# Performance work log

Measured on AMD Instinct MI355X. Metric: run time of the kernel, lower is better.

## Reference

```python
import jax, jax.numpy as jnp
import numpy as np

HEAD_DIM = 64
AGGR = 4  # attn_aggr_ratio
BN_EPS = 1e-5


def _conv1x1(x, W, b=None):
    # x: [N, Cin, L], W: [Cout, Cin] -> [N, Cout, L]
    y = jnp.einsum('ncl,oc->nol', x, W)
    if b is not None:
        y = y + b[None, :, None]
    return y


def _bn(x, gamma, beta, mean, var):
    # BatchNorm1d, eval mode (running stats). x: [N, C, L]
    inv = gamma * jax.lax.rsqrt(var + BN_EPS)
    return x * inv[None, :, None] + (beta - mean * inv)[None, :, None]


def setup_inputs() -> dict:
    key = jax.random.key(0)
    ks = jax.random.split(key, 8)
    N, C, L = 4, 256, 4096
    s = 1.0 / np.sqrt(C)
    inp = {
        'x': jax.random.normal(ks[0], (N, C, L), jnp.float32),
        'Wq': jax.random.normal(ks[1], (C, C), jnp.float32) * s,
        'bq': jnp.zeros((C,), jnp.float32),
        'Wk': jax.random.normal(ks[2], (C, C), jnp.float32) * s,
        'bk': jnp.zeros((C,), jnp.float32),
        'Wv': jax.random.normal(ks[3], (C, C), jnp.float32) * s,
        'bv': jnp.zeros((C,), jnp.float32),
        'Wo': jax.random.normal(ks[4], (C, C), jnp.float32) * s,
        'bo': jnp.zeros((C,), jnp.float32),
        'Wa': jax.random.normal(ks[5], (C, C), jnp.float32) * s,
        'g1': jnp.ones((C,), jnp.float32), 'b1': jnp.zeros((C,), jnp.float32),
        'm1': jnp.zeros((C,), jnp.float32), 'v1': jnp.ones((C,), jnp.float32),
        'g2': jnp.ones((C,), jnp.float32), 'b2': jnp.zeros((C,), jnp.float32),
        'm2': jnp.zeros((C,), jnp.float32), 'v2': jnp.ones((C,), jnp.float32),
    }
    return inp


def reference(x, Wq, bq, Wk, bk, Wv, bv, Wo, bo, Wa,
              g1, b1, m1, v1, g2, b2, m2, v2):
    N, C, L = x.shape
    H, E = C // HEAD_DIM, HEAD_DIM
    # q projection on full-resolution input
    q = _conv1x1(x, Wq, bq).reshape(N, H, E, L)
    # LocalAwareAggregationBlock: avg+max pool (kernel=AGGR, L divisible), 1x1 conv, BN
    xp = x.reshape(N, C, L // AGGR, AGGR)
    xa = xp.mean(axis=-1) + xp.max(axis=-1)          # [N, C, L//AGGR]
    xa = _conv1x1(xa, Wa)                             # bias=False
    xa = _bn(xa, g1, b1, m1, v1)
    # post-aggregation norm
    xa = _bn(xa, g2, b2, m2, v2)
    k = _conv1x1(xa, Wk, bk).reshape(N, H, E, -1)     # [N, H, E, L2]
    v = _conv1x1(xa, Wv, bv).reshape(N, H, E, -1)
    # attention: softmax((q/sqrt(E))^T k) @ v^T
    scale = 1.0 / np.sqrt(E)
    scores = jnp.einsum('nhel,nhem->nhlm', q * scale, k)  # [N, H, L, L2]
    attn = jax.nn.softmax(scores, axis=-1)
    o = jnp.einsum('nhlm,nhem->nhel', attn, v).reshape(N, C, L)
    return _conv1x1(o, Wo, bo)
```

## Files before the change

### kernel.cpp

```cpp
#include <hip/hip_runtime.h>
#include <stdint.h>

constexpr int NBATCH = 4;
constexpr int CH     = 256;
constexpr int LEN    = 4096;
constexpr int LPOOL  = 1024;
constexpr int NH     = 4;
constexpr int HD     = 64;

typedef __attribute__((ext_vector_type(8))) short short8;
typedef __attribute__((ext_vector_type(4))) float float4e;
typedef __attribute__((ext_vector_type(16))) float float16e;
typedef __attribute__((ext_vector_type(2))) unsigned uint2v;

__device__ __forceinline__ unsigned short f2bf(float f) {
    union { unsigned int i; float f; } v; v.f = f;
    unsigned int lsb = (v.i >> 16) & 1u;
    v.i += 0x7fffu + lsb;
    return (unsigned short)(v.i >> 16);
}
__device__ __forceinline__ unsigned pack2bf(float lo, float hi) {
    unsigned a = __float_as_uint(lo) + 0x8000u;
    unsigned b = __float_as_uint(hi) + 0x8000u;
    return __builtin_amdgcn_perm(b, a, 0x07060302u);
}
__device__ __forceinline__ float fast_exp2(float x) {
#if __has_builtin(__builtin_amdgcn_exp2f)
    return __builtin_amdgcn_exp2f(x);
#else
    float r;
    asm("v_exp_f32 %0, %1" : "=v"(r) : "v"(x));
    return r;
#endif
}
__device__ __forceinline__ void gload16(const void* g, void* l) {
    __builtin_amdgcn_global_load_lds(
        (const __attribute__((address_space(1))) unsigned int*)g,
        (__attribute__((address_space(3))) unsigned int*)l, 16, 0, 0);
}

__global__ __launch_bounds__(256) void transpool_setup(
    const float* __restrict__ x, unsigned short* __restrict__ xbf,
    unsigned short* __restrict__ poolT,
    const float* __restrict__ w0, const float* __restrict__ w1,
    const float* __restrict__ w2, const float* __restrict__ w3,
    const float* __restrict__ w4, unsigned short* __restrict__ outW,
    const float* __restrict__ g1, const float* __restrict__ b1,
    const float* __restrict__ m1, const float* __restrict__ v1,
    const float* __restrict__ g2, const float* __restrict__ b2,
    const float* __restrict__ m2, const float* __restrict__ v2,
    float* __restrict__ scale, float* __restrict__ shift,
    const float* __restrict__ bk, const float* __restrict__ bv,
    float* __restrict__ bkv)
{
    __shared__ float T[64][65];
    __shared__ float P16[64][17];
    int b = blockIdx.x, t = threadIdx.x;
    if (b >= 1024) {
        int sb = b - 1024;
        if (sb < 320) {
            int gid = sb * 256 + t;
            int w = gid >> 14;
            int off = (gid & 16383) * 4;
            const float* src = (w == 0) ? w0 : (w == 1) ? w1 : (w == 2) ? w2 : (w == 3) ? w3 : w4;
            float4 v = *(const float4*)(src + off);
            uint2 pk;
            pk.x = pack2bf(v.x, v.y);
            pk.y = pack2bf(v.z, v.w);
            *(uint2*)(outW + w * 65536 + off) = pk;
        } else {
            float inv1 = g1[t] * rsqrtf(v1[t] + 1e-5f);
            float inv2 = g2[t] * rsqrtf(v2[t] + 1e-5f);
            scale[t] = inv1 * inv2;
            shift[t] = (b1[t] - m1[t] * inv1) * inv2 + (b2[t] - m2[t] * inv2);
            bkv[t] = bk[t];
            bkv[256 + t] = bv[t];
        }
        return;
    }
    int n = b >> 8, c0 = ((b >> 6) & 3) * 64, l0 = (b & 63) * 64;
    const float* xp = x + ((size_t)n * CH + c0) * LEN + l0;
    #pragma unroll
    for (int i = 0; i < 4; i++) {
        int idx = t + i * 256;
        int c = idx >> 4, l4 = idx & 15;
        float4 v = *(const float4*)(xp + (size_t)c * LEN + l4 * 4);
        T[c][l4 * 4 + 0] = v.x; T[c][l4 * 4 + 1] = v.y;
        T[c][l4 * 4 + 2] = v.z; T[c][l4 * 4 + 3] = v.w;
        P16[c][l4] = (v.x + v.y + v.z + v.w) * 0.25f
                   + fmaxf(fmaxf(v.x, v.y), fmaxf(v.z, v.w));
    }
    __syncthreads();
    unsigned short* op = xbf + ((size_t)n * LEN + l0) * CH + c0;
    #pragma unroll
    for (int i = 0; i < 4; i++) {
        int idx = t + i * 256;
        int l = idx >> 4, c4 = idx & 15;
        uint2 pk;
        pk.x = pack2bf(T[c4 * 4 + 0][l], T[c4 * 4 + 1][l]);
        pk.y = pack2bf(T[c4 * 4 + 2][l], T[c4 * 4 + 3][l]);
        *(uint2*)(op + (size_t)l * CH + c4 * 4) = pk;
    }
    int p0 = l0 >> 2;
    #pragma unroll
    for (int k = 0; k < 2; k++) {
        int p = (t >> 5) + k * 8;
        int c2 = (t & 31) * 2;
        unsigned pk = pack2bf(P16[c2][p], P16[c2 + 1][p]);
        *(unsigned*)(poolT + ((size_t)n * LPOOL + p0 + p) * CH + c0 + c2) = pk;
    }
}

__global__ __launch_bounds__(256, 4) void gemm_mfma(
    const unsigned short* __restrict__ A,
    const unsigned short* __restrict__ B, size_t bBatch,
    const float* __restrict__ biasRow,
    const float* __restrict__ scale, const float* __restrict__ shift,
    float* __restrict__ outF, size_t oFBatch,
    unsigned short* __restrict__ out1, size_t o1Batch, int cs1,
    unsigned short* __restrict__ out2, size_t o2Batch, int rs2, int rowSplit,
    int NN, float outScale)
{
    __shared__ unsigned short As[2][64 * 64];
    __shared__ unsigned short Bs[2][64 * 64];

    int n = blockIdx.z;
    int t = threadIdx.x;
    int wave = t >> 6, lane = t & 63, m = lane & 15, quad = lane >> 4;
    int wm = wave & 1, wn = wave >> 1;
    int rowTile = blockIdx.y * 64;
    int col0 = blockIdx.x * 64;

    const unsigned short* Ab = A + (size_t)rowTile * 256;
    const unsigned short* Bb = B + (size_t)n * bBatch + (size_t)col0 * 256;

    float4e acc[2][2] = {};

    int srow[2], sch[2], ldsW[2];
    #pragma unroll
    for (int i = 0; i < 2; i++) {
        int idx = t + i * 256;
        srow[i] = idx >> 3;
        sch[i]  = idx & 7;
        ldsW[i] = wave * 1024 + i * 4096;
    }

    int aoff[2][2], boff[2][2];
    #pragma unroll
    for (int i = 0; i < 2; i++) {
        int ra = wm * 32 + i * 16 + m;
        int rb = wn * 32 + i * 16 + m;
        #pragma unroll
        for (int kc = 0; kc < 2; kc++) {
            aoff[i][kc] = ra * 128 + kc * 64 + quad * 16;
            boff[i][kc] = rb * 128 + kc * 64 + quad * 16;
        }
    }

    #pragma unroll
    for (int i = 0; i < 2; i++) {
        gload16(Ab + (size_t)srow[i] * 256 + sch[i] * 8, (char*)As[0] + ldsW[i]);
        gload16(Bb + (size_t)srow[i] * 256 + sch[i] * 8, (char*)Bs[0] + ldsW[i]);
    }

    #pragma unroll
    for (int s = 0; s < 4; s++) {
        int cur = s & 1;
        asm volatile("s_waitcnt vmcnt(0)" ::: "memory");
        __builtin_amdgcn_sched_barrier(0);
        __builtin_amdgcn_s_barrier();
        __builtin_amdgcn_sched_barrier(0);
        if (s < 3) {
            int nxt = cur ^ 1;
            int kk = (s + 1) * 64;
            #pragma unroll
            for (int i = 0; i < 2; i++) {
                gload16(Ab + (size_t)srow[i] * 256 + kk + sch[i] * 8, (char*)As[nxt] + ldsW[i]);
                gload16(Bb + (size_t)srow[i] * 256 + kk + sch[i] * 8, (char*)Bs[nxt] + ldsW[i]);
            }
        }
        const char* AsC = (const char*)As[cur];
        const char* BsC = (const char*)Bs[cur];
        #pragma unroll
        for (int kc = 0; kc < 2; kc++) {
            short8 af[2], bfr[2];
            #pragma unroll
            for (int i = 0; i < 2; i++) {
                af[i]  = *(const short8*)(AsC + aoff[i][kc]);
                bfr[i] = *(const short8*)(BsC + boff[i][kc]);
            }
            __builtin_amdgcn_s_setprio(1);
            #pragma unroll
            for (int i = 0; i < 2; i++)
                #pragma unroll
                for (int j = 0; j < 2; j++)
                    acc[i][j] = __builtin_amdgcn_mfma_f32_16x16x32_bf16(af[i], bfr[j], acc[i][j], 0, 0, 0);
            __builtin_amdgcn_s_setprio(0);
        }
    }
    __syncthreads();

    if (outF) {
        float* TOf = (float*)Bs;
        float* dst = outF + (size_t)n * oFBatch;
        #pragma unroll
        for (int i = 0; i < 2; i++) {
            int rowL = wm * 32 + i * 16 + quad * 4;
            int rowG = rowTile + rowL;
            float br[4], sc[4], sh[4];
            #pragma unroll
            for (int r = 0; r < 4; r++) {
                br[r] = biasRow ? biasRow[rowG + r] : 0.0f;
                sc[r] = scale ? scale[rowG + r] : 1.0f;
                sh[r] = shift ? shift[rowG + r] : 0.0f;
            }
            #pragma unroll
            for (int j = 0; j < 2; j++) {
                int colL = wn * 32 + j * 16 + m;
                float4e c = acc[i][j];
                #pragma unroll
                for (int r = 0; r < 4; r++)
                    TOf[(rowL + r) * 64 + colL] = ((c[r] + br[r]) * sc[r] + sh[r]) * outScale;
            }
        }
        __syncthreads();
        #pragma unroll
        for (int w = 0; w < 4; w++) {
            int idx = t + w * 256;
            int row = idx >> 4, c4 = idx & 15;
            *(float4*)(dst + (size_t)(rowTile + row) * NN + col0 + c4 * 4) =
                *(const float4*)&TOf[row * 64 + c4 * 4];
        }
        return;
    }

    bool mode2 = (rowTile >= rowSplit);
    unsigned short* TO = (unsigned short*)Bs;
    #pragma unroll
    for (int i = 0; i < 2; i++) {
        int rowL = wm * 32 + i * 16 + quad * 4;
        int rowG = rowTile + rowL;
        float br[4], sc[4], sh[4];
        #pragma unroll
        for (int r = 0; r < 4; r++) {
            br[r] = biasRow ? biasRow[rowG + r] : 0.0f;
            sc[r] = scale ? scale[rowG + r] : 1.0f;
            sh[r] = shift ? shift[rowG + r] : 0.0f;
        }
        #pragma unroll
        for (int j = 0; j < 2; j++) {
            int colL = wn * 32 + j * 16 + m;
            float4e c = acc[i][j];
            float v0 = ((c[0] + br[0]) * sc[0] + sh[0]) * outScale;
            float v1 = ((c[1] + br[1]) * sc[1] + sh[1]) * outScale;
            float v2 = ((c[2] + br[2]) * sc[2] + sh[2]) * outScale;
            float v3 = ((c[3] + br[3]) * sc[3] + sh[3]) * outScale;
            if (!mode2) {
                uint2 pk;
                pk.x = pack2bf(v0, v1);
                pk.y = pack2bf(v2, v3);
                *(uint2*)&TO[colL * 72 + rowL] = pk;
            } else {
                TO[(rowL + 0) * 72 + colL] = f2bf(v0);
                TO[(rowL + 1) * 72 + colL] = f2bf(v1);
                TO[(rowL + 2) * 72 + colL] = f2bf(v2);
                TO[(rowL + 3) * 72 + colL] = f2bf(v3);
            }
        }
    }
    __syncthreads();
    if (!mode2) {
        unsigned short* dst = out1 + (size_t)n * o1Batch;
        #pragma unroll
        for (int w = 0; w < 2; w++) {
            int idx = t + w * 256;
            int l = idx >> 3, ch = idx & 7;
            *(uint4*)(dst + (size_t)(col0 + l) * cs1 + rowTile + ch * 8) =
                *(const uint4*)&TO[l * 72 + ch * 8];
        }
    } else {
        unsigned short* dst = out2 + (size_t)n * o2Batch;
        int rowBase = rowTile - rowSplit;
        #pragma unroll
        for (int w = 0; w < 2; w++) {
            int idx = t + w * 256;
            int row = idx >> 3, ch = idx & 7;
            *(uint4*)(dst + (size_t)(rowBase + row) * rs2 + col0 + ch * 8) =
                *(const uint4*)&TO[row * 72 + ch * 8];
        }
    }
}

__global__ __launch_bounds__(256, 2) void attn_mfma(
    const unsigned short* __restrict__ Qb,
    const unsigned short* __restrict__ Kb,
    const unsigned short* __restrict__ Vb,
    unsigned short* __restrict__ Obf)
{
    __shared__ unsigned short Ks[2][64 * 64];
    __shared__ unsigned short Vs[2][64 * 64];

    int qb = blockIdx.x;
    int h  = blockIdx.y;
    int n  = blockIdx.z;
    int t  = threadIdx.x;
    int wave = t >> 6, lane = t & 63;
    int col = lane & 31;
    int hi  = lane >> 5;
    int l0 = qb * 128 + wave * 32;

    const unsigned short* qp = Qb + ((size_t)n * LEN + l0 + col) * CH + h * HD + hi * 8;
    short8 bQ[4];
    #pragma unroll
    for (int dc = 0; dc < 4; dc++)
        bQ[dc] = *(const short8*)(qp + dc * 16);

    float16e Oa[2];
    #pragma unroll
    for (int e = 0; e < 2; e++)
        #pragma unroll
        for (int r = 0; r < 16; r++) Oa[e][r] = 0.0f;
    float l_run = 0.0f;

    const unsigned short* KgBase = Kb + (size_t)n * LPOOL * CH + h * HD;
    const unsigned short* VgBase = Vb + ((size_t)n * CH + h * HD) * LPOOL;
    const float NEG = -17.312340f;

    int srow[2], schs[2], ldsb[2];
    #pragma unroll
    for (int i = 0; i < 2; i++) {
        int idx = t + i * 256;
        srow[i] = idx >> 3;
        schs[i] = (idx & 7) ^ (srow[i] & 7);
        ldsb[i] = wave * 1024 + i * 4096;
    }
    int ldoff[2][4];
    #pragma unroll
    for (int g = 0; g < 2; g++)
        #pragma unroll
        for (int c = 0; c < 4; c++) {
            int row = g * 32 + col;
            ldoff[g][c] = row * 128 + ((c * 32 + hi * 16) ^ ((row & 7) << 4));
        }

    #pragma unroll
    for (int i = 0; i < 2; i++) {
        gload16(KgBase + (size_t)srow[i] * CH + schs[i] * 8, (char*)Ks[0] + ldsb[i]);
        gload16(VgBase + (size_t)srow[i] * LPOOL + schs[i] * 8, (char*)Vs[0] + ldsb[i]);
    }

    #pragma unroll 2
    for (int kt = 0; kt < 16; kt++) {
        int cur = kt & 1;
        asm volatile("s_waitcnt vmcnt(0)" ::: "memory");
        __builtin_amdgcn_sched_barrier(0);
        __builtin_amdgcn_s_barrier();
        __builtin_amdgcn_sched_barrier(0);
        if (kt < 15) {
            int nxt = cur ^ 1;
            const unsigned short* ksrc = KgBase + (size_t)(kt + 1) * 64 * CH;
            const unsigned short* vsrc = VgBase + (kt + 1) * 64;
            #pragma unroll
            for (int i = 0; i < 2; i++) {
                gload16(ksrc + (size_t)srow[i] * CH + schs[i] * 8, (char*)Ks[nxt] + ldsb[i]);
                gload16(vsrc + (size_t)srow[i] * LPOOL + schs[i] * 8, (char*)Vs[nxt] + ldsb[i]);
            }
        }

        const char* KsC = (const char*)Ks[cur];
        const char* VsC = (const char*)Vs[cur];
        #pragma unroll
        for (int kh = 0; kh < 2; kh++) {
            float16e c;
            #pragma unroll
            for (int r = 0; r < 16; r++) c[r] = NEG;
            __builtin_amdgcn_s_setprio(1);
            #pragma unroll
            for (int dc = 0; dc < 4; dc++) {
                short8 a = *(const short8*)(KsC + ldoff[kh][dc]);
                c = __builtin_amdgcn_mfma_f32_32x32x16_bf16(a, bQ[dc], c, 0, 0, 0);
            }
            __builtin_amdgcn_s_setprio(0);
            float p[16];
            #pragma unroll
            for (int r = 0; r < 16; r++) p[r] = fast_exp2(c[r]);
            l_run += ((p[0] + p[1]) + (p[2] + p[3])) + ((p[4] + p[5]) + (p[6] + p[7]))
                   + ((p[8] + p[9]) + (p[10] + p[11])) + ((p[12] + p[13]) + (p[14] + p[15]));
            union { unsigned u[4]; short8 s; } bP[2];
            #pragma unroll
            for (int kc2 = 0; kc2 < 2; kc2++) {
                int rb = kc2 * 8;
                unsigned A0 = pack2bf(p[rb + 0], p[rb + 1]);
                unsigned B0 = pack2bf(p[rb + 4], p[rb + 5]);
                unsigned A1 = pack2bf(p[rb + 2], p[rb + 3]);
                unsigned B1 = pack2bf(p[rb + 6], p[rb + 7]);
                uint2v s0 = __builtin_amdgcn_permlane32_swap(A0, B0, false, false);
                uint2v s1 = __builtin_amdgcn_permlane32_swap(A1, B1, false, false);
                bP[kc2].u[0] = s0[0];
                bP[kc2].u[1] = s1[0];
                bP[kc2].u[2] = s0[1];
                bP[kc2].u[3] = s1[1];
            }
            __builtin_amdgcn_s_setprio(1);
            #pragma unroll
            for (int eh = 0; eh < 2; eh++)
                #pragma unroll
                for (int kc2 = 0; kc2 < 2; kc2++) {
                    short8 av = *(const short8*)(VsC + ldoff[eh][kh * 2 + kc2]);
                    Oa[eh] = __builtin_amdgcn_mfma_f32_32x32x16_bf16(av, bP[kc2].s, Oa[eh], 0, 0, 0);
                }
            __builtin_amdgcn_s_setprio(0);
        }
    }

    float l = l_run + __shfl_xor(l_run, 32);
    float inv = 1.0f / l;
    unsigned short* op = Obf + ((size_t)n * LEN + l0 + col) * CH + h * HD + hi * 4;
    #pragma unroll
    for (int eh = 0; eh < 2; eh++)
        #pragma unroll
        for (int rq = 0; rq < 4; rq++) {
            int r = rq * 4;
            uint2 pk;
            pk.x = pack2bf(Oa[eh][r + 0] * inv, Oa[eh][r + 1] * inv);
            pk.y = pack2bf(Oa[eh][r + 2] * inv, Oa[eh][r + 3] * inv);
            *(uint2*)(op + eh * 32 + rq * 8) = pk;
        }
}

extern "C" void kernel_launch(void* const* d_in, const int* in_sizes, int n_in,
                              void* d_out, int out_size, void* d_ws, size_t ws_size,
                              hipStream_t stream)
{
    const float* x  = (const float*)d_in[0];
    const float* Wq = (const float*)d_in[1];
    const float* bq = (const float*)d_in[2];
    const float* Wk = (const float*)d_in[3];
    const float* bk = (const float*)d_in[4];
    const float* Wv = (const float*)d_in[5];
    const float* bv = (const float*)d_in[6];
    const float* Wo = (const float*)d_in[7];
    const float* bo = (const float*)d_in[8];
    const float* Wa = (const float*)d_in[9];
    const float* g1 = (const float*)d_in[10];
    const float* b1 = (const float*)d_in[11];
    const float* m1 = (const float*)d_in[12];
    const float* v1 = (const float*)d_in[13];
    const float* g2 = (const float*)d_in[14];
    const float* b2 = (const float*)d_in[15];
    const float* m2 = (const float*)d_in[16];
    const float* v2 = (const float*)d_in[17];

    float* wsf      = (float*)d_ws;
    float* bn_scale = wsf;
    float* bn_shift = wsf + 256;
    float* bkv      = wsf + 512;
    unsigned short* Wbf   = (unsigned short*)(wsf + 1024);
    unsigned short* xbf   = Wbf + 5 * 65536;
    unsigned short* poolT = xbf   + (size_t)NBATCH * LEN * CH;
    unsigned short* xabf  = poolT + (size_t)NBATCH * LPOOL * CH;
    unsigned short* Kbf   = xabf  + (size_t)NBATCH * LPOOL * CH;
    unsigned short* Vbf   = Kbf   + (size_t)NBATCH * LPOOL * CH;
    unsigned short* Qbf   = Vbf   + (size_t)NBATCH * LPOOL * CH;
    unsigned short* Obf   = Qbf   + (size_t)NBATCH * LEN * CH;

    transpool_setup<<<1345, 256, 0, stream>>>(x, xbf, poolT,
        Wq, Wk, Wv, Wo, Wa, Wbf,
        g1, b1, m1, v1, g2, b2, m2, v2, bn_scale, bn_shift, bk, bv, bkv);

    gemm_mfma<<<dim3(64, 4, 4), 256, 0, stream>>>(
        Wbf + 0 * 65536, xbf, (size_t)LEN * CH, bq, nullptr, nullptr,
        nullptr, 0, Qbf, (size_t)LEN * CH, 256, nullptr, 0, 0, 1 << 30,
        LEN, 0.18033688f);

    gemm_mfma<<<dim3(16, 4, 4), 256, 0, stream>>>(
        Wbf + 4 * 65536, poolT, (size_t)LPOOL * CH, nullptr, bn_scale, bn_shift,
        nullptr, 0, xabf, (size_t)LPOOL * CH, 256, nullptr, 0, 0, 1 << 30,
        LPOOL, 1.0f);

    gemm_mfma<<<dim3(16, 8, 4), 256, 0, stream>>>(
        Wbf + 1 * 65536, xabf, (size_t)LPOOL * CH, bkv, nullptr, nullptr,
        nullptr, 0, Kbf, (size_t)LPOOL * CH, 256, Vbf, (size_t)LPOOL * CH, LPOOL, 256,
        LPOOL, 1.0f);

    attn_mfma<<<dim3(LEN / 128, NH, NBATCH), 256, 0, stream>>>(Qbf, Kbf, Vbf, Obf);

    gemm_mfma<<<dim3(64, 4, 4), 256, 0, stream>>>(
        Wbf + 3 * 65536, Obf, (size_t)LEN * CH, bo, nullptr, nullptr,
        (float*)d_out, (size_t)CH * LEN, nullptr, 0, 0, nullptr, 0, 0, 1 << 30,
        LEN, 1.0f);
}
```

Before: 156.9 us.

## Fuse all stages into one persistent kernel with atomic grid barriers

```diff
diff --git a/kernel.cpp b/kernel.cpp
--- a/kernel.cpp
+++ b/kernel.cpp
@@ -7,6 +7,7 @@
 constexpr int LPOOL  = 1024;
 constexpr int NH     = 4;
 constexpr int HD     = 64;
+constexpr int NBLK   = 512;
 
 typedef __attribute__((ext_vector_type(8))) short short8;
 typedef __attribute__((ext_vector_type(4))) float float4e;
@@ -39,7 +40,19 @@
         (__attribute__((address_space(3))) unsigned int*)l, 16, 0, 0);
 }
 
-__global__ __launch_bounds__(256) void transpool_setup(
+__device__ __forceinline__ void gbar(unsigned* cnt, unsigned target) {
+    __threadfence();
+    __syncthreads();
+    if (threadIdx.x == 0) {
+        __hip_atomic_fetch_add(cnt, 1u, __ATOMIC_RELEASE, __HIP_MEMORY_SCOPE_AGENT);
+        while (__hip_atomic_load(cnt, __ATOMIC_ACQUIRE, __HIP_MEMORY_SCOPE_AGENT) < target)
+            __builtin_amdgcn_s_sleep(8);
+    }
+    __syncthreads();
+}
+
+__device__ __forceinline__ void transpool_block(
+    int b, char* smemc,
     const float* __restrict__ x, unsigned short* __restrict__ xbf,
     unsigned short* __restrict__ poolT,
     const float* __restrict__ w0, const float* __restrict__ w1,
@@ -53,9 +66,9 @@
     const float* __restrict__ bk, const float* __restrict__ bv,
     float* __restrict__ bkv)
 {
-    __shared__ float T[64][65];
-    __shared__ float P16[64][17];
-    int b = blockIdx.x, t = threadIdx.x;
+    float* T  = (float*)smemc;
+    float* P16 = (float*)(smemc + 16640);
+    int t = threadIdx.x;
     if (b >= 1024) {
         int sb = b - 1024;
         if (sb < 320) {
@@ -85,10 +98,10 @@
         int idx = t + i * 256;
         int c = idx >> 4, l4 = idx & 15;
         float4 v = *(const float4*)(xp + (size_t)c * LEN + l4 * 4);
-        T[c][l4 * 4 + 0] = v.x; T[c][l4 * 4 + 1] = v.y;
-        T[c][l4 * 4 + 2] = v.z; T[c][l4 * 4 + 3] = v.w;
-        P16[c][l4] = (v.x + v.y + v.z + v.w) * 0.25f
-                   + fmaxf(fmaxf(v.x, v.y), fmaxf(v.z, v.w));
+        T[c * 65 + l4 * 4 + 0] = v.x; T[c * 65 + l4 * 4 + 1] = v.y;
+        T[c * 65 + l4 * 4 + 2] = v.z; T[c * 65 + l4 * 4 + 3] = v.w;
+        P16[c * 17 + l4] = (v.x + v.y + v.z + v.w) * 0.25f
+                         + fmaxf(fmaxf(v.x, v.y), fmaxf(v.z, v.w));
     }
     __syncthreads();
     unsigned short* op = xbf + ((size_t)n * LEN + l0) * CH + c0;
@@ -97,8 +110,8 @@
         int idx = t + i * 256;
         int l = idx >> 4, c4 = idx & 15;
         uint2 pk;
-        pk.x = pack2bf(T[c4 * 4 + 0][l], T[c4 * 4 + 1][l]);
-        pk.y = pack2bf(T[c4 * 4 + 2][l], T[c4 * 4 + 3][l]);
+        pk.x = pack2bf(T[(c4 * 4 + 0) * 65 + l], T[(c4 * 4 + 1) * 65 + l]);
+        pk.y = pack2bf(T[(c4 * 4 + 2) * 65 + l], T[(c4 * 4 + 3) * 65 + l]);
         *(uint2*)(op + (size_t)l * CH + c4 * 4) = pk;
     }
     int p0 = l0 >> 2;
@@ -106,12 +119,13 @@
     for (int k = 0; k < 2; k++) {
         int p = (t >> 5) + k * 8;
         int c2 = (t & 31) * 2;
-        unsigned pk = pack2bf(P16[c2][p], P16[c2 + 1][p]);
+        unsigned pk = pack2bf(P16[c2 * 17 + p], P16[(c2 + 1) * 17 + p]);
         *(unsigned*)(poolT + ((size_t)n * LPOOL + p0 + p) * CH + c0 + c2) = pk;
     }
 }
 
-__global__ __launch_bounds__(256, 4) void gemm_mfma(
+__device__ __forceinline__ void gemm_block(
+    int bx, int by, int bz, char* smemc,
     const unsigned short* __restrict__ A,
     const unsigned short* __restrict__ B, size_t bBatch,
     const float* __restrict__ biasRow,
@@ -121,15 +135,15 @@
     unsigned short* __restrict__ out2, size_t o2Batch, int rs2, int rowSplit,
     int NN, float outScale)
 {
-    __shared__ unsigned short As[2][64 * 64];
-    __shared__ unsigned short Bs[2][64 * 64];
-
-    int n = blockIdx.z;
+    char* AsB[2] = { smemc,         smemc + 8192 };
+    char* BsB[2] = { smemc + 16384, smemc + 24576 };
+
+    int n = bz;
     int t = threadIdx.x;
     int wave = t >> 6, lane = t & 63, m = lane & 15, quad = lane >> 4;
     int wm = wave & 1, wn = wave >> 1;
-    int rowTile = blockIdx.y * 64;
-    int col0 = blockIdx.x * 64;
+    int rowTile = by * 64;
+    int col0 = bx * 64;
 
     const unsigned short* Ab = A + (size_t)rowTile * 256;
     const unsigned short* Bb = B + (size_t)n * bBatch + (size_t)col0 * 256;
@@ -144,7 +158,6 @@
         sch[i]  = idx & 7;
         ldsW[i] = wave * 1024 + i * 4096;
     }
-
     int aoff[2][2], boff[2][2];
     #pragma unroll
     for (int i = 0; i < 2; i++) {
@@ -159,8 +172,8 @@
 
     #pragma unroll
     for (int i = 0; i < 2; i++) {
-        gload16(Ab + (size_t)srow[i] * 256 + sch[i] * 8, (char*)As[0] + ldsW[i]);
-        gload16(Bb + (size_t)srow[i] * 256 + sch[i] * 8, (char*)Bs[0] + ldsW[i]);
+        gload16(Ab + (size_t)srow[i] * 256 + sch[i] * 8, AsB[0] + ldsW[i]);
+        gload16(Bb + (size_t)srow[i] * 256 + sch[i] * 8, BsB[0] + ldsW[i]);
     }
 
     #pragma unroll
@@ -175,12 +188,12 @@
             int kk = (s + 1) * 64;
             #pragma unroll
             for (int i = 0; i < 2; i++) {
-                gload16(Ab + (size_t)srow[i] * 256 + kk + sch[i] * 8, (char*)As[nxt] + ldsW[i]);
-                gload16(Bb + (size_t)srow[i] * 256 + kk + sch[i] * 8, (char*)Bs[nxt] + ldsW[i]);
-            }
-        }
-        const char* AsC = (const char*)As[cur];
-        const char* BsC = (const char*)Bs[cur];
+                gload16(Ab + (size_t)srow[i] * 256 + kk + sch[i] * 8, AsB[nxt] + ldsW[i]);
+                gload16(Bb + (size_t)srow[i] * 256 + kk + sch[i] * 8, BsB[nxt] + ldsW[i]);
+            }
+        }
+        const char* AsC = AsB[cur];
+        const char* BsC = BsB[cur];
         #pragma unroll
         for (int kc = 0; kc < 2; kc++) {
             short8 af[2], bfr[2];
@@ -201,7 +214,7 @@
     __syncthreads();
 
     if (outF) {
-        float* TOf = (float*)Bs;
+        float* TOf = (float*)BsB[0];
         float* dst = outF + (size_t)n * oFBatch;
         #pragma unroll
         for (int i = 0; i < 2; i++) {
@@ -235,7 +248,7 @@
     }
 
     bool mode2 = (rowTile >= rowSplit);
-    unsigned short* TO = (unsigned short*)Bs;
+    unsigned short* TO = (unsigned short*)BsB[0];
     #pragma unroll
     for (int i = 0; i < 2; i++) {
         int rowL = wm * 32 + i * 16 + quad * 4;
@@ -291,18 +304,16 @@
     }
 }
 
-__global__ __launch_bounds__(256, 2) void attn_mfma(
+__device__ __forceinline__ void attn_block(
+    int qb, int h, int n, char* smemc,
     const unsigned short* __restrict__ Qb,
     const unsigned short* __restrict__ Kb,
     const unsigned short* __restrict__ Vb,
     unsigned short* __restrict__ Obf)
 {
-    __shared__ unsigned short Ks[2][64 * 64];
-    __shared__ unsigned short Vs[2][64 * 64];
-
-    int qb = blockIdx.x;
-    int h  = blockIdx.y;
-    int n  = blockIdx.z;
+    char* KsB[2] = { smemc,         smemc + 8192 };
+    char* VsB[2] = { smemc + 16384, smemc + 24576 };
+
     int t  = threadIdx.x;
     int wave = t >> 6, lane = t & 63;
     int col = lane & 31;
@@ -345,8 +356,8 @@
 
     #pragma unroll
     for (int i = 0; i < 2; i++) {
-        gload16(KgBase + (size_t)srow[i] * CH + schs[i] * 8, (char*)Ks[0] + ldsb[i]);
-        gload16(VgBase + (size_t)srow[i] * LPOOL + schs[i] * 8, (char*)Vs[0] + ldsb[i]);
+        gload16(KgBase + (size_t)srow[i] * CH + schs[i] * 8, KsB[0] + ldsb[i]);
+        gload16(VgBase + (size_t)srow[i] * LPOOL + schs[i] * 8, VsB[0] + ldsb[i]);
     }
 
     #pragma unroll 2
@@ -362,13 +373,13 @@
             const unsigned short* vsrc = VgBase + (kt + 1) * 64;
             #pragma unroll
             for (int i = 0; i < 2; i++) {
-                gload16(ksrc + (size_t)srow[i] * CH + schs[i] * 8, (char*)Ks[nxt] + ldsb[i]);
-                gload16(vsrc + (size_t)srow[i] * LPOOL + schs[i] * 8, (char*)Vs[nxt] + ldsb[i]);
-            }
-        }
-
-        const char* KsC = (const char*)Ks[cur];
-        const char* VsC = (const char*)Vs[cur];
+                gload16(ksrc + (size_t)srow[i] * CH + schs[i] * 8, KsB[nxt] + ldsb[i]);
+                gload16(vsrc + (size_t)srow[i] * LPOOL + schs[i] * 8, VsB[nxt] + ldsb[i]);
+            }
+        }
+
+        const char* KsC = KsB[cur];
+        const char* VsC = VsB[cur];
         #pragma unroll
         for (int kh = 0; kh < 2; kh++) {
             float16e c;
@@ -426,6 +437,80 @@
             pk.y = pack2bf(Oa[eh][r + 2] * inv, Oa[eh][r + 3] * inv);
             *(uint2*)(op + eh * 32 + rq * 8) = pk;
         }
+}
+
+__global__ __launch_bounds__(256, 2) void mega(
+    const float* __restrict__ x,
+    const float* __restrict__ Wq, const float* __restrict__ bq,
+    const float* __restrict__ Wk, const float* __restrict__ bk,
+    const float* __restrict__ Wv, const float* __restrict__ bv,
+    const float* __restrict__ Wo, const float* __restrict__ bo,
+    const float* __restrict__ Wa,
+    const float* __restrict__ g1, const float* __restrict__ b1,
+    const float* __restrict__ m1, const float* __restrict__ v1,
+    const float* __restrict__ g2, const float* __restrict__ b2,
+    const float* __restrict__ m2, const float* __restrict__ v2,
+    float* __restrict__ bn_scale, float* __restrict__ bn_shift,
+    float* __restrict__ bkv,
+    unsigned short* __restrict__ Wbf, unsigned short* __restrict__ xbf,
+    unsigned short* __restrict__ poolT, unsigned short* __restrict__ xabf,
+    unsigned short* __restrict__ Kbf, unsigned short* __restrict__ Vbf,
+    unsigned short* __restrict__ Qbf, unsigned short* __restrict__ Obf,
+    float* __restrict__ outp, unsigned* __restrict__ gcnt)
+{
+    __shared__ __align__(16) char smem[32768];
+    int bid = blockIdx.x;
+
+    for (int b = bid; b < 1345; b += NBLK) {
+        __syncthreads();
+        transpool_block(b, smem, x, xbf, poolT, Wq, Wk, Wv, Wo, Wa, Wbf,
+                        g1, b1, m1, v1, g2, b2, m2, v2,
+                        bn_scale, bn_shift, bk, bv, bkv);
+    }
+    gbar(gcnt, NBLK);
+
+    for (int vb = bid; vb < 1280; vb += NBLK) {
+        __syncthreads();
+        if (vb < 1024) {
+            int bx = vb & 63, by = (vb >> 6) & 3, bz = vb >> 8;
+            gemm_block(bx, by, bz, smem, Wbf + 0 * 65536, xbf, (size_t)LEN * CH,
+                       bq, nullptr, nullptr, nullptr, 0,
+                       Qbf, (size_t)LEN * CH, 256, nullptr, 0, 0, 1 << 30,
+                       LEN, 0.18033688f);
+        } else {
+            int v2b = vb - 1024;
+            int bx = v2b & 15, by = (v2b >> 4) & 3, bz = v2b >> 6;
+            gemm_block(bx, by, bz, smem, Wbf + 4 * 65536, poolT, (size_t)LPOOL * CH,
+                       nullptr, bn_scale, bn_shift, nullptr, 0,
+                       xabf, (size_t)LPOOL * CH, 256, nullptr, 0, 0, 1 << 30,
+                       LPOOL, 1.0f);
+        }
+    }
+    gbar(gcnt, 2 * NBLK);
+
+    {
+        int bx = bid & 15, by = (bid >> 4) & 7, bz = bid >> 7;
+        gemm_block(bx, by, bz, smem, Wbf + 1 * 65536, xabf, (size_t)LPOOL * CH,
+                   bkv, nullptr, nullptr, nullptr, 0,
+                   Kbf, (size_t)LPOOL * CH, 256, Vbf, (size_t)LPOOL * CH, LPOOL, 256,
+                   LPOOL, 1.0f);
+    }
+    gbar(gcnt, 3 * NBLK);
+
+    {
+        int qb = bid & 31, h = (bid >> 5) & 3, n = bid >> 7;
+        attn_block(qb, h, n, smem, Qbf, Kbf, Vbf, Obf);
+    }
+    gbar(gcnt, 4 * NBLK);
+
+    for (int vb = bid; vb < 1024; vb += NBLK) {
+        __syncthreads();
+        int bx = vb & 63, by = (vb >> 6) & 3, bz = vb >> 8;
+        gemm_block(bx, by, bz, smem, Wbf + 3 * 65536, Obf, (size_t)LEN * CH,
+                   bo, nullptr, nullptr, outp, (size_t)CH * LEN,
+                   nullptr, 0, 0, nullptr, 0, 0, 1 << 30,
+                   LEN, 1.0f);
+    }
 }
 
 extern "C" void kernel_launch(void* const* d_in, const int* in_sizes, int n_in,
@@ -463,30 +548,13 @@
     unsigned short* Vbf   = Kbf   + (size_t)NBATCH * LPOOL * CH;
     unsigned short* Qbf   = Vbf   + (size_t)NBATCH * LPOOL * CH;
     unsigned short* Obf   = Qbf   + (size_t)NBATCH * LEN * CH;
-
-    transpool_setup<<<1345, 256, 0, stream>>>(x, xbf, poolT,
-        Wq, Wk, Wv, Wo, Wa, Wbf,
-        g1, b1, m1, v1, g2, b2, m2, v2, bn_scale, bn_shift, bk, bv, bkv);
-
-    gemm_mfma<<<dim3(64, 4, 4), 256, 0, stream>>>(
-        Wbf + 0 * 65536, xbf, (size_t)LEN * CH, bq, nullptr, nullptr,
-        nullptr, 0, Qbf, (size_t)LEN * CH, 256, nullptr, 0, 0, 1 << 30,
-        LEN, 0.18033688f);
-
-    gemm_mfma<<<dim3(16, 4, 4), 256, 0, stream>>>(
-        Wbf + 4 * 65536, poolT, (size_t)LPOOL * CH, nullptr, bn_scale, bn_shift,
-        nullptr, 0, xabf, (size_t)LPOOL * CH, 256, nullptr, 0, 0, 1 << 30,
-        LPOOL, 1.0f);
-
-    gemm_mfma<<<dim3(16, 8, 4), 256, 0, stream>>>(
-        Wbf + 1 * 65536, xabf, (size_t)LPOOL * CH, bkv, nullptr, nullptr,
-        nullptr, 0, Kbf, (size_t)LPOOL * CH, 256, Vbf, (size_t)LPOOL * CH, LPOOL, 256,
-        LPOOL, 1.0f);
-
-    attn_mfma<<<dim3(LEN / 128, NH, NBATCH), 256, 0, stream>>>(Qbf, Kbf, Vbf, Obf);
-
-    gemm_mfma<<<dim3(64, 4, 4), 256, 0, stream>>>(
-        Wbf + 3 * 65536, Obf, (size_t)LEN * CH, bo, nullptr, nullptr,
-        (float*)d_out, (size_t)CH * LEN, nullptr, 0, 0, nullptr, 0, 0, 1 << 30,
-        LEN, 1.0f);
-}
+    unsigned* gcnt = (unsigned*)(Obf + (size_t)NBATCH * LEN * CH);
+
+    hipMemsetAsync(gcnt, 0, sizeof(unsigned), stream);
+    mega<<<NBLK, 256, 0, stream>>>(
+        x, Wq, bq, Wk, bk, Wv, bv, Wo, bo, Wa,
+        g1, b1, m1, v1, g2, b2, m2, v2,
+        bn_scale, bn_shift, bkv,
+        Wbf, xbf, poolT, xabf, Kbf, Vbf, Qbf, Obf,
+        (float*)d_out, gcnt);
+}
```

Result: slower. 524.3 us (+234.2%).

## Merge Q and aggregation GEMMs into one launch; triple-buffer attention K/V tiles

Applied to the files above, without the earlier changes.

```diff
diff --git a/kernel.cpp b/kernel.cpp
--- a/kernel.cpp
+++ b/kernel.cpp
@@ -39,7 +39,8 @@
         (__attribute__((address_space(3))) unsigned int*)l, 16, 0, 0);
 }
 
-__global__ __launch_bounds__(256) void transpool_setup(
+__device__ __forceinline__ void transpool_block(
+    int b, char* smemc,
     const float* __restrict__ x, unsigned short* __restrict__ xbf,
     unsigned short* __restrict__ poolT,
     const float* __restrict__ w0, const float* __restrict__ w1,
@@ -53,9 +54,9 @@
     const float* __restrict__ bk, const float* __restrict__ bv,
     float* __restrict__ bkv)
 {
-    __shared__ float T[64][65];
-    __shared__ float P16[64][17];
-    int b = blockIdx.x, t = threadIdx.x;
+    float* T   = (float*)smemc;
+    float* P16 = (float*)(smemc + 16640);
+    int t = threadIdx.x;
     if (b >= 1024) {
         int sb = b - 1024;
         if (sb < 320) {
@@ -85,10 +86,10 @@
         int idx = t + i * 256;
         int c = idx >> 4, l4 = idx & 15;
         float4 v = *(const float4*)(xp + (size_t)c * LEN + l4 * 4);
-        T[c][l4 * 4 + 0] = v.x; T[c][l4 * 4 + 1] = v.y;
-        T[c][l4 * 4 + 2] = v.z; T[c][l4 * 4 + 3] = v.w;
-        P16[c][l4] = (v.x + v.y + v.z + v.w) * 0.25f
-                   + fmaxf(fmaxf(v.x, v.y), fmaxf(v.z, v.w));
+        T[c * 65 + l4 * 4 + 0] = v.x; T[c * 65 + l4 * 4 + 1] = v.y;
+        T[c * 65 + l4 * 4 + 2] = v.z; T[c * 65 + l4 * 4 + 3] = v.w;
+        P16[c * 17 + l4] = (v.x + v.y + v.z + v.w) * 0.25f
+                         + fmaxf(fmaxf(v.x, v.y), fmaxf(v.z, v.w));
     }
     __syncthreads();
     unsigned short* op = xbf + ((size_t)n * LEN + l0) * CH + c0;
@@ -97,8 +98,8 @@
         int idx = t + i * 256;
         int l = idx >> 4, c4 = idx & 15;
         uint2 pk;
-        pk.x = pack2bf(T[c4 * 4 + 0][l], T[c4 * 4 + 1][l]);
-        pk.y = pack2bf(T[c4 * 4 + 2][l], T[c4 * 4 + 3][l]);
+        pk.x = pack2bf(T[(c4 * 4 + 0) * 65 + l], T[(c4 * 4 + 1) * 65 + l]);
+        pk.y = pack2bf(T[(c4 * 4 + 2) * 65 + l], T[(c4 * 4 + 3) * 65 + l]);
         *(uint2*)(op + (size_t)l * CH + c4 * 4) = pk;
     }
     int p0 = l0 >> 2;
@@ -106,12 +107,32 @@
     for (int k = 0; k < 2; k++) {
         int p = (t >> 5) + k * 8;
         int c2 = (t & 31) * 2;
-        unsigned pk = pack2bf(P16[c2][p], P16[c2 + 1][p]);
+        unsigned pk = pack2bf(P16[c2 * 17 + p], P16[(c2 + 1) * 17 + p]);
         *(unsigned*)(poolT + ((size_t)n * LPOOL + p0 + p) * CH + c0 + c2) = pk;
     }
 }
 
-__global__ __launch_bounds__(256, 4) void gemm_mfma(
+__global__ __launch_bounds__(256) void transpool_setup(
+    const float* __restrict__ x, unsigned short* __restrict__ xbf,
+    unsigned short* __restrict__ poolT,
+    const float* __restrict__ w0, const float* __restrict__ w1,
+    const float* __restrict__ w2, const float* __restrict__ w3,
+    const float* __restrict__ w4, unsigned short* __restrict__ outW,
+    const float* __restrict__ g1, const float* __restrict__ b1,
+    const float* __restrict__ m1, const float* __restrict__ v1,
+    const float* __restrict__ g2, const float* __restrict__ b2,
+    const float* __restrict__ m2, const float* __restrict__ v2,
+    float* __restrict__ scale, float* __restrict__ shift,
+    const float* __restrict__ bk, const float* __restrict__ bv,
+    float* __restrict__ bkv)
+{
+    __shared__ __align__(16) char smem[20992];
+    transpool_block(blockIdx.x, smem, x, xbf, poolT, w0, w1, w2, w3, w4, outW,
+                    g1, b1, m1, v1, g2, b2, m2, v2, scale, shift, bk, bv, bkv);
+}
+
+__device__ __forceinline__ void gemm_block(
+    int bx, int by, int bz, char* smemc,
     const unsigned short* __restrict__ A,
     const unsigned short* __restrict__ B, size_t bBatch,
     const float* __restrict__ biasRow,
@@ -121,15 +142,15 @@
     unsigned short* __restrict__ out2, size_t o2Batch, int rs2, int rowSplit,
     int NN, float outScale)
 {
-    __shared__ unsigned short As[2][64 * 64];
-    __shared__ unsigned short Bs[2][64 * 64];
-
-    int n = blockIdx.z;
+    char* AsB[2] = { smemc,         smemc + 8192 };
+    char* BsB[2] = { smemc + 16384, smemc + 24576 };
+
+    int n = bz;
     int t = threadIdx.x;
     int wave = t >> 6, lane = t & 63, m = lane & 15, quad = lane >> 4;
     int wm = wave & 1, wn = wave >> 1;
-    int rowTile = blockIdx.y * 64;
-    int col0 = blockIdx.x * 64;
+    int rowTile = by * 64;
+    int col0 = bx * 64;
 
     const unsigned short* Ab = A + (size_t)rowTile * 256;
     const unsigned short* Bb = B + (size_t)n * bBatch + (size_t)col0 * 256;
@@ -144,7 +165,6 @@
         sch[i]  = idx & 7;
         ldsW[i] = wave * 1024 + i * 4096;
     }
-
     int aoff[2][2], boff[2][2];
     #pragma unroll
     for (int i = 0; i < 2; i++) {
@@ -159,8 +179,8 @@
 
     #pragma unroll
     for (int i = 0; i < 2; i++) {
-        gload16(Ab + (size_t)srow[i] * 256 + sch[i] * 8, (char*)As[0] + ldsW[i]);
-        gload16(Bb + (size_t)srow[i] * 256 + sch[i] * 8, (char*)Bs[0] + ldsW[i]);
+        gload16(Ab + (size_t)srow[i] * 256 + sch[i] * 8, AsB[0] + ldsW[i]);
+        gload16(Bb + (size_t)srow[i] * 256 + sch[i] * 8, BsB[0] + ldsW[i]);
     }
 
     #pragma unroll
@@ -175,12 +195,12 @@
             int kk = (s + 1) * 64;
             #pragma unroll
             for (int i = 0; i < 2; i++) {
-                gload16(Ab + (size_t)srow[i] * 256 + kk + sch[i] * 8, (char*)As[nxt] + ldsW[i]);
-                gload16(Bb + (size_t)srow[i] * 256 + kk + sch[i] * 8, (char*)Bs[nxt] + ldsW[i]);
-            }
-        }
-        const char* AsC = (const char*)As[cur];
-        const char* BsC = (const char*)Bs[cur];
+                gload16(Ab + (size_t)srow[i] * 256 + kk + sch[i] * 8, AsB[nxt] + ldsW[i]);
+                gload16(Bb + (size_t)srow[i] * 256 + kk + sch[i] * 8, BsB[nxt] + ldsW[i]);
+            }
+        }
+        const char* AsC = AsB[cur];
+        const char* BsC = BsB[cur];
         #pragma unroll
         for (int kc = 0; kc < 2; kc++) {
             short8 af[2], bfr[2];
@@ -201,7 +221,7 @@
     __syncthreads();
 
     if (outF) {
-        float* TOf = (float*)Bs;
+        float* TOf = (float*)BsB[0];
         float* dst = outF + (size_t)n * oFBatch;
         #pragma unroll
         for (int i = 0; i < 2; i++) {
@@ -235,7 +255,7 @@
     }
 
     bool mode2 = (rowTile >= rowSplit);
-    unsigned short* TO = (unsigned short*)Bs;
+    unsigned short* TO = (unsigned short*)BsB[0];
     #pragma unroll
     for (int i = 0; i < 2; i++) {
         int rowL = wm * 32 + i * 16 + quad * 4;
@@ -291,14 +311,52 @@
     }
 }
 
+__global__ __launch_bounds__(256, 4) void gemm_single(
+    const unsigned short* __restrict__ A,
+    const unsigned short* __restrict__ B, size_t bBatch,
+    const float* __restrict__ biasRow,
+    const float* __restrict__ scale, const float* __restrict__ shift,
+    float* __restrict__ outF, size_t oFBatch,
+    unsigned short* __restrict__ out1, size_t o1Batch, int cs1,
+    unsigned short* __restrict__ out2, size_t o2Batch, int rs2, int rowSplit,
+    int NN, float outScale)
+{
+    __shared__ __align__(16) char smem[32768];
+    gemm_block(blockIdx.x, blockIdx.y, blockIdx.z, smem, A, B, bBatch,
+               biasRow, scale, shift, outF, oFBatch,
+               out1, o1Batch, cs1, out2, o2Batch, rs2, rowSplit, NN, outScale);
+}
+
+__global__ __launch_bounds__(256, 4) void gemm_qxa(
+    const unsigned short* __restrict__ Wqbf, const unsigned short* __restrict__ xbf,
+    const float* __restrict__ bq, unsigned short* __restrict__ Qbf,
+    const unsigned short* __restrict__ Wabf, const unsigned short* __restrict__ poolT,
+    const float* __restrict__ bn_scale, const float* __restrict__ bn_shift,
+    unsigned short* __restrict__ xabf)
+{
+    __shared__ __align__(16) char smem[32768];
+    int bx = blockIdx.x;
+    if (bx < 64) {
+        gemm_block(bx, blockIdx.y, blockIdx.z, smem, Wqbf, xbf, (size_t)LEN * CH,
+                   bq, nullptr, nullptr, nullptr, 0,
+                   Qbf, (size_t)LEN * CH, 256, nullptr, 0, 0, 1 << 30,
+                   LEN, 0.18033688f);
+    } else {
+        gemm_block(bx - 64, blockIdx.y, blockIdx.z, smem, Wabf, poolT, (size_t)LPOOL * CH,
+                   nullptr, bn_scale, bn_shift, nullptr, 0,
+                   xabf, (size_t)LPOOL * CH, 256, nullptr, 0, 0, 1 << 30,
+                   LPOOL, 1.0f);
+    }
+}
+
 __global__ __launch_bounds__(256, 2) void attn_mfma(
     const unsigned short* __restrict__ Qb,
     const unsigned short* __restrict__ Kb,
     const unsigned short* __restrict__ Vb,
     unsigned short* __restrict__ Obf)
 {
-    __shared__ unsigned short Ks[2][64 * 64];
-    __shared__ unsigned short Vs[2][64 * 64];
+    __shared__ unsigned short Ks[3][64 * 64];
+    __shared__ unsigned short Vs[3][64 * 64];
 
     int qb = blockIdx.x;
     int h  = blockIdx.y;
@@ -343,32 +401,18 @@
             ldoff[g][c] = row * 128 + ((c * 32 + hi * 16) ^ ((row & 7) << 4));
         }
 
-    #pragma unroll
-    for (int i = 0; i < 2; i++) {
-        gload16(KgBase + (size_t)srow[i] * CH + schs[i] * 8, (char*)Ks[0] + ldsb[i]);
-        gload16(VgBase + (size_t)srow[i] * LPOOL + schs[i] * 8, (char*)Vs[0] + ldsb[i]);
-    }
-
-    #pragma unroll 2
-    for (int kt = 0; kt < 16; kt++) {
-        int cur = kt & 1;
-        asm volatile("s_waitcnt vmcnt(0)" ::: "memory");
-        __builtin_amdgcn_sched_barrier(0);
-        __builtin_amdgcn_s_barrier();
-        __builtin_amdgcn_sched_barrier(0);
-        if (kt < 15) {
-            int nxt = cur ^ 1;
-            const unsigned short* ksrc = KgBase + (size_t)(kt + 1) * 64 * CH;
-            const unsigned short* vsrc = VgBase + (kt + 1) * 64;
-            #pragma unroll
-            for (int i = 0; i < 2; i++) {
-                gload16(ksrc + (size_t)srow[i] * CH + schs[i] * 8, (char*)Ks[nxt] + ldsb[i]);
-                gload16(vsrc + (size_t)srow[i] * LPOOL + schs[i] * 8, (char*)Vs[nxt] + ldsb[i]);
-            }
-        }
-
-        const char* KsC = (const char*)Ks[cur];
-        const char* VsC = (const char*)Vs[cur];
+    auto issue_tile = [&](int tile, int buf) {
+        const unsigned short* ksrc = KgBase + (size_t)tile * 64 * CH;
+        const unsigned short* vsrc = VgBase + tile * 64;
+        #pragma unroll
+        for (int i = 0; i < 2; i++)
+            gload16(ksrc + (size_t)srow[i] * CH + schs[i] * 8, (char*)Ks[buf] + ldsb[i]);
+        #pragma unroll
+        for (int i = 0; i < 2; i++)
+            gload16(vsrc + (size_t)srow[i] * LPOOL + schs[i] * 8, (char*)Vs[buf] + ldsb[i]);
+    };
+
+    auto tile_compute = [&](const char* KsC, const char* VsC) {
         #pragma unroll
         for (int kh = 0; kh < 2; kh++) {
             float16e c;
@@ -411,7 +455,30 @@
                 }
             __builtin_amdgcn_s_setprio(0);
         }
-    }
+    };
+
+    issue_tile(0, 0);
+    issue_tile(1, 1);
+
+    int cur = 0;
+    #pragma unroll 3
+    for (int kt = 0; kt < 15; kt++) {
+        asm volatile("s_waitcnt vmcnt(4)" ::: "memory");
+        __builtin_amdgcn_sched_barrier(0);
+        __builtin_amdgcn_s_barrier();
+        __builtin_amdgcn_sched_barrier(0);
+        if (kt < 14) {
+            int nb = cur - 1; if (nb < 0) nb = 2;
+            issue_tile(kt + 2, nb);
+        }
+        tile_compute((const char*)Ks[cur], (const char*)Vs[cur]);
+        cur = (cur == 2) ? 0 : cur + 1;
+    }
+    asm volatile("s_waitcnt vmcnt(0)" ::: "memory");
+    __builtin_amdgcn_sched_barrier(0);
+    __builtin_amdgcn_s_barrier();
+    __builtin_amdgcn_sched_barrier(0);
+    tile_compute((const char*)Ks[cur], (const char*)Vs[cur]);
 
     float l = l_run + __shfl_xor(l_run, 32);
     float inv = 1.0f / l;
@@ -468,24 +535,18 @@
         Wq, Wk, Wv, Wo, Wa, Wbf,
         g1, b1, m1, v1, g2, b2, m2, v2, bn_scale, bn_shift, bk, bv, bkv);
 
-    gemm_mfma<<<dim3(64, 4, 4), 256, 0, stream>>>(
-        Wbf + 0 * 65536, xbf, (size_t)LEN * CH, bq, nullptr, nullptr,
-        nullptr, 0, Qbf, (size_t)LEN * CH, 256, nullptr, 0, 0, 1 << 30,
-        LEN, 0.18033688f);
-
-    gemm_mfma<<<dim3(16, 4, 4), 256, 0, stream>>>(
-        Wbf + 4 * 65536, poolT, (size_t)LPOOL * CH, nullptr, bn_scale, bn_shift,
-        nullptr, 0, xabf, (size_t)LPOOL * CH, 256, nullptr, 0, 0, 1 << 30,
-        LPOOL, 1.0f);
-
-    gemm_mfma<<<dim3(16, 8, 4), 256, 0, stream>>>(
+    gemm_qxa<<<dim3(80, 4, 4), 256, 0, stream>>>(
+        Wbf + 0 * 65536, xbf, bq, Qbf,
+        Wbf + 4 * 65536, poolT, bn_scale, bn_shift, xabf);
+
+    gemm_single<<<dim3(16, 8, 4), 256, 0, stream>>>(
         Wbf + 1 * 65536, xabf, (size_t)LPOOL * CH, bkv, nullptr, nullptr,
         nullptr, 0, Kbf, (size_t)LPOOL * CH, 256, Vbf, (size_t)LPOOL * CH, LPOOL, 256,
         LPOOL, 1.0f);
 
     attn_mfma<<<dim3(LEN / 128, NH, NBATCH), 256, 0, stream>>>(Qbf, Kbf, Vbf, Obf);
 
-    gemm_mfma<<<dim3(64, 4, 4), 256, 0, stream>>>(
+    gemm_single<<<dim3(64, 4, 4), 256, 0, stream>>>(
         Wbf + 3 * 65536, Obf, (size_t)LEN * CH, bo, nullptr, nullptr,
         (float*)d_out, (size_t)CH * LEN, nullptr, 0, 0, nullptr, 0, 0, 1 << 30,
         LEN, 1.0f);
```

After: 151.9 us. 3.2% less time.
